# Kernel optimization log

Measured on AMD Instinct MI355X. Metric: run time of the kernel, lower is better.

The kernel has to match this reference:

```python
import jax, jax.numpy as jnp
import numpy as np

N, E, D_IN, HID, H = 50000, 800000, 128, 64, 2
C = HID  # per-head dim (out_channels)


def _lin_params(key, fan_in, fan_out):
    kw, kb = jax.random.split(key)
    s = 1.0 / np.sqrt(fan_in)
    W = jax.random.uniform(kw, (fan_in, fan_out), jnp.float32, -s, s)
    b = jax.random.uniform(kb, (fan_out,), jnp.float32, -s, s)
    return W, b


def setup_inputs() -> dict:
    key = jax.random.key(0)
    ks = jax.random.split(key, 14)
    x = jax.random.normal(ks[0], (N, D_IN), jnp.float32)
    edge_index = jax.random.randint(ks[1], (2, E), 0, N, jnp.int32)
    inp = {"x": x, "edge_index": edge_index}
    dims = [D_IN, HID, HID]
    i = 2
    for L, d_in in enumerate(dims, start=1):
        for nm, fo in (("q", H * C), ("k", H * C), ("v", H * C), ("s", HID)):
            W, b = _lin_params(ks[i], d_in, fo)
            inp[f"W{L}{nm}"] = W
            inp[f"b{L}{nm}"] = b
            i += 1
            if i >= 14:
                ks = jax.random.split(ks[-1], 14)
                i = 0
    return inp


def _transformer_conv(x, src, dst, Wq, bq, Wk, bk, Wv, bv, Ws, bs):
    # x: [N, d_in] -> out: [N, HID]
    q = (x @ Wq + bq).reshape(N, H, C)
    k = (x @ Wk + bk).reshape(N, H, C)
    v = (x @ Wv + bv).reshape(N, H, C)
    qi = q[dst]                      # [E, H, C] gather at destination (query)
    kj = k[src]                      # [E, H, C] gather at source (key)
    alpha = jnp.sum(qi * kj, axis=-1) / jnp.sqrt(jnp.float32(C))  # [E, H]
    amax = jax.ops.segment_max(alpha, dst, num_segments=N)        # [N, H]
    ex = jnp.exp(alpha - amax[dst])                               # [E, H]
    denom = jax.ops.segment_sum(ex, dst, num_segments=N)          # [N, H]
    attn = ex / (denom[dst] + 1e-16)                              # [E, H]
    msg = v[src] * attn[:, :, None]                               # [E, H, C]
    out = jax.ops.segment_sum(msg, dst, num_segments=N)           # [N, H, C]
    out = out.mean(axis=1)                                        # concat=False: head mean
    return out + x @ Ws + bs                                      # root skip


def reference(x, edge_index,
              W1q, b1q, W1k, b1k, W1v, b1v, W1s, b1s,
              W2q, b2q, W2k, b2k, W2v, b2v, W2s, b2s,
              W3q, b3q, W3k, b3k, W3v, b3v, W3s, b3s):
    src, dst = edge_index[0], edge_index[1]
    h = jax.nn.relu(_transformer_conv(x, src, dst, W1q, b1q, W1k, b1k, W1v, b1v, W1s, b1s))
    h = jax.nn.relu(_transformer_conv(h, src, dst, W2q, b2q, W2k, b2k, W2v, b2v, W2s, b2s))
    h = jax.nn.relu(_transformer_conv(h, src, dst, W3q, b3q, W3k, b3k, W3v, b3v, W3s, b3s))
    return h
```

## Files before the change

### kernel.cpp

```cpp
#include <hip/hip_runtime.h>
#include <cstdint>

typedef _Float16 f16;
typedef __attribute__((ext_vector_type(2))) _Float16 f16x2;
typedef __attribute__((ext_vector_type(4))) _Float16 f16x4;
typedef __attribute__((ext_vector_type(8))) _Float16 f16x8;
typedef __attribute__((ext_vector_type(4))) float f32x4;

#if defined(__has_builtin)
# if __has_builtin(__builtin_amdgcn_fdot2)
#  define HAVE_FDOT2 1
# endif
#endif


__global__ void hist_kernel(const int* __restrict__ dst, int* __restrict__ cnt, int E) {
    int e = blockIdx.x * blockDim.x + threadIdx.x;
    if (e < E) atomicAdd(&cnt[dst[e]], 1);
}

__global__ __launch_bounds__(256) void block_scan_kernel(
    const int* __restrict__ cnt, int* __restrict__ rowptr,
    int* __restrict__ partials, int n) {
    __shared__ int lds[256];
    int tid = threadIdx.x;
    int i = blockIdx.x * 256 + tid;
    int v = (i < n) ? cnt[i] : 0;
    lds[tid] = v;
    __syncthreads();
    for (int off = 1; off < 256; off <<= 1) {
        int t = (tid >= off) ? lds[tid - off] : 0;
        __syncthreads();
        lds[tid] += t;
        __syncthreads();
    }
    if (i < n) rowptr[i + 1] = lds[tid];
    if (tid == 255) partials[blockIdx.x] = lds[255];
}

__global__ __launch_bounds__(256) void partial_scan_kernel(int* __restrict__ partials, int nb) {
    __shared__ int lds[256];
    int tid = threadIdx.x;
    int v = (tid < nb) ? partials[tid] : 0;
    lds[tid] = v;
    __syncthreads();
    for (int off = 1; off < 256; off <<= 1) {
        int t = (tid >= off) ? lds[tid - off] : 0;
        __syncthreads();
        lds[tid] += t;
        __syncthreads();
    }
    if (tid < nb) partials[tid] = lds[tid] - v;
}

__global__ __launch_bounds__(256) void add_offsets_kernel(
    int* __restrict__ rowptr, const int* __restrict__ partials, int n) {
    int i = blockIdx.x * 256 + threadIdx.x;
    if (i < n) rowptr[i + 1] += partials[blockIdx.x];
    if (i == 0) rowptr[0] = 0;
}

__global__ void scatter_kernel(const int* __restrict__ src, const int* __restrict__ dst,
                               const int* __restrict__ rowptr, int* __restrict__ cnt,
                               int* __restrict__ src_sorted, int E) {
    int e = blockIdx.x * blockDim.x + threadIdx.x;
    if (e < E) {
        int d = dst[e];
        int p = rowptr[d] + atomicAdd(&cnt[d], 1);
        src_sorted[p] = src[e];
    }
}


__global__ __launch_bounds__(256) void prep_w_kernel(
    const float* __restrict__ Wq, const float* __restrict__ Wk,
    const float* __restrict__ Wv, const float* __restrict__ Ws,
    const float* __restrict__ bq, const float* __restrict__ bk,
    const float* __restrict__ bv, const float* __restrict__ bs,
    f16* __restrict__ Wt, float* __restrict__ bias, int K) {
    int idx = blockIdx.x * 256 + threadIdx.x;
    if (idx < 448) {
        bias[idx] = (idx < 128) ? bq[idx]
                  : (idx < 256) ? bk[idx - 128]
                  : (idx < 384) ? bv[idx - 256]
                  : bs[idx - 384];
    }
    if (idx >= 448 * K) return;
    int c = idx / K, k = idx - c * K;
    float v;
    if (c < 128)      v = Wq[k * 128 + c];
    else if (c < 256) v = Wk[k * 128 + (c - 128)];
    else if (c < 384) v = Wv[k * 128 + (c - 256)];
    else              v = Ws[k * 64 + (c - 384)];
    Wt[(size_t)c * K + k] = (f16)v;
}


template <int K, bool F32IN>
__global__ __launch_bounds__(256) void gemm_qkvs_kernel(
    const void* __restrict__ Xv, const f16* __restrict__ Wt,
    const float* __restrict__ bias, f16* __restrict__ out, int M) {
    __shared__ f16 xa[64 * K];
    __shared__ f16 wb[2][64 * K];
    int row0 = blockIdx.x * 64;
    int tid = threadIdx.x;
    constexpr int CPRW = K / 8;

    if (F32IN) {
        const float* X = (const float*)Xv;
        constexpr int CPR = K / 4;
        for (int c = tid; c < 64 * CPR; c += 256) {
            int r = c / CPR, kc = c % CPR;
            int gr = row0 + r;
            float4 v = {0.f, 0.f, 0.f, 0.f};
            if (gr < M) v = *(const float4*)(X + (size_t)gr * K + kc * 4);
            f16x4 hv = {(f16)v.x, (f16)v.y, (f16)v.z, (f16)v.w};
            int off = (r * K + kc * 4) * 2;
            off ^= (r & 7) << 4;
            *(f16x4*)((char*)xa + off) = hv;
        }
    } else {
        const f16* X = (const f16*)Xv;
        for (int c = tid; c < 64 * CPRW; c += 256) {
            int r = c / CPRW, kc = c % CPRW;
            int gr = row0 + r;
            uint4 v = {0, 0, 0, 0};
            if (gr < M) v = *(const uint4*)(X + (size_t)gr * K + kc * 8);
            int off = (r * K + kc * 8) * 2;
            off ^= (r & 7) << 4;
            *(uint4*)((char*)xa + off) = v;
        }
    }
    for (int c = tid; c < 64 * CPRW; c += 256) {
        int r = c / CPRW, kc = c % CPRW;
        uint4 v = *(const uint4*)(Wt + (size_t)r * K + kc * 8);
        int off = (r * K + kc * 8) * 2;
        off ^= (r & 7) << 4;
        *(uint4*)((char*)wb[0] + off) = v;
    }
    __syncthreads();

    int lane = tid & 63, wid = tid >> 6;
    int fr = lane & 15, fk = lane >> 4;
    int arow = wid * 16 + fr;
    constexpr int NK = K / 32;
    f16x8 af[NK];
    #pragma unroll
    for (int ks = 0; ks < NK; ++ks) {
        int aoff = (arow * K + ks * 32 + fk * 8) * 2;
        aoff ^= (arow & 7) << 4;
        af[ks] = *(f16x8*)((char*)xa + aoff);
    }

    int orow = row0 + wid * 16 + fk * 4;
    for (int ct = 0; ct < 7; ++ct) {
        if (ct < 6) {
            int col0 = (ct + 1) * 64;
            f16* dstb = wb[(ct + 1) & 1];
            for (int c = tid; c < 64 * CPRW; c += 256) {
                int r = c / CPRW, kc = c % CPRW;
                uint4 v = *(const uint4*)(Wt + (size_t)(col0 + r) * K + kc * 8);
                int off = (r * K + kc * 8) * 2;
                off ^= (r & 7) << 4;
                *(uint4*)((char*)dstb + off) = v;
            }
        }

        const f16* curb = wb[ct & 1];
        f32x4 acc[4] = {};
        #pragma unroll
        for (int ks = 0; ks < NK; ++ks) {
            #pragma unroll
            for (int cf = 0; cf < 4; ++cf) {
                int brow = cf * 16 + fr;
                int boff = (brow * K + ks * 32 + fk * 8) * 2;
                boff ^= (brow & 7) << 4;
                f16x8 bf = *(f16x8*)((char*)curb + boff);
                acc[cf] = __builtin_amdgcn_mfma_f32_16x16x32_f16(af[ks], bf, acc[cf], 0, 0, 0);
            }
        }

        int ocol = ct * 64 + fr;
        #pragma unroll
        for (int cf = 0; cf < 4; ++cf) {
            float b = bias[ocol + cf * 16];
            #pragma unroll
            for (int r = 0; r < 4; ++r) {
                int gr = orow + r;
                if (gr < M) out[(size_t)gr * 448 + ocol + cf * 16] = (f16)(acc[cf][r] + b);
            }
        }
        __syncthreads();
    }
}


__global__ __launch_bounds__(256) void attn_kernel(
    const f16* __restrict__ T,
    const int* __restrict__ rowptr, const int* __restrict__ srcs,
    f16* __restrict__ hout, float* __restrict__ fout, int n, int final_layer) {
    int node = blockIdx.x * 4 + (threadIdx.x >> 6);
    if (node >= n) return;
    int lane = threadIdx.x & 63;
    int c8 = lane & 7, eg = lane >> 3;
    const size_t base = (size_t)node * 448;
    const int co = c8 * 8;

    f16x8 q0 = *(const f16x8*)(T + base + co);
    f16x8 q1 = *(const f16x8*)(T + base + 64 + co);
    float m0 = -__builtin_inff(), m1 = -__builtin_inff();
    float s0 = 0.f, s1 = 0.f;
    float av0[8] = {}, av1[8] = {};

    int beg = rowptr[node], end = rowptr[node + 1];
    if (beg < end) {
        int nsrc = srcs[min(beg + eg, end - 1)];
        for (int i0 = beg; i0 < end; i0 += 8) {
            int i = i0 + eg;
            bool valid = (i < end);
            int sidx = nsrc;
            if (i0 + 8 < end) nsrc = srcs[min(i + 8, end - 1)];

            const f16* p = T + (size_t)sidx * 448 + co;
            f16x8 k0 = *(const f16x8*)(p + 128);
            f16x8 k1 = *(const f16x8*)(p + 192);
            f16x8 v0 = *(const f16x8*)(p + 256);
            f16x8 v1 = *(const f16x8*)(p + 320);

            float d0 = 0.f, d1 = 0.f;
#ifdef HAVE_FDOT2
            #pragma unroll
            for (int j = 0; j < 4; ++j) {
                f16x2 a0 = {q0[2 * j], q0[2 * j + 1]};
                f16x2 b0 = {k0[2 * j], k0[2 * j + 1]};
                d0 = __builtin_amdgcn_fdot2(a0, b0, d0, false);
                f16x2 a1 = {q1[2 * j], q1[2 * j + 1]};
                f16x2 b1 = {k1[2 * j], k1[2 * j + 1]};
                d1 = __builtin_amdgcn_fdot2(a1, b1, d1, false);
            }
#else
            #pragma unroll
            for (int j = 0; j < 8; ++j) {
                d0 += (float)q0[j] * (float)k0[j];
                d1 += (float)q1[j] * (float)k1[j];
            }
#endif
            d0 += __shfl_xor(d0, 1); d1 += __shfl_xor(d1, 1);
            d0 += __shfl_xor(d0, 2); d1 += __shfl_xor(d1, 2);
            d0 += __shfl_xor(d0, 4); d1 += __shfl_xor(d1, 4);
            d0 *= 0.125f; d1 *= 0.125f;
            if (!valid) { d0 = -__builtin_inff(); d1 = -__builtin_inff(); }

            if (__any(d0 > m0 + 6.f || d1 > m1 + 6.f)) {
                float t0 = d0, t1 = d1;
                t0 = fmaxf(t0, __shfl_xor(t0, 8));  t1 = fmaxf(t1, __shfl_xor(t1, 8));
                t0 = fmaxf(t0, __shfl_xor(t0, 16)); t1 = fmaxf(t1, __shfl_xor(t1, 16));
                t0 = fmaxf(t0, __shfl_xor(t0, 32)); t1 = fmaxf(t1, __shfl_xor(t1, 32));
                float nm0 = fmaxf(m0, t0), nm1 = fmaxf(m1, t1);
                float f0 = __expf(m0 - nm0), f1 = __expf(m1 - nm1);
                s0 *= f0; s1 *= f1;
                #pragma unroll
                for (int j = 0; j < 8; ++j) { av0[j] *= f0; av1[j] *= f1; }
                m0 = nm0; m1 = nm1;
            }
            float p0 = __expf(d0 - m0);
            float p1 = __expf(d1 - m1);
            s0 += p0; s1 += p1;
            #pragma unroll
            for (int j = 0; j < 8; ++j) {
                av0[j] += p0 * (float)v0[j];
                av1[j] += p1 * (float)v1[j];
            }
        }
    }

    s0 += __shfl_xor(s0, 8);  s1 += __shfl_xor(s1, 8);
    s0 += __shfl_xor(s0, 16); s1 += __shfl_xor(s1, 16);
    s0 += __shfl_xor(s0, 32); s1 += __shfl_xor(s1, 32);
    float inv0 = 1.0f / (s0 + 1e-16f), inv1 = 1.0f / (s1 + 1e-16f);
    float r[8];
    #pragma unroll
    for (int j = 0; j < 8; ++j) {
        float a0 = av0[j], a1 = av1[j];
        a0 += __shfl_xor(a0, 8);  a1 += __shfl_xor(a1, 8);
        a0 += __shfl_xor(a0, 16); a1 += __shfl_xor(a1, 16);
        a0 += __shfl_xor(a0, 32); a1 += __shfl_xor(a1, 32);
        r[j] = 0.5f * (a0 * inv0 + a1 * inv1);
    }

    if (lane < 8) {
        f16x8 sk = *(const f16x8*)(T + base + 384 + co);
        #pragma unroll
        for (int j = 0; j < 8; ++j) r[j] = fmaxf(r[j] + (float)sk[j], 0.f);
        if (final_layer) {
            float4* dst4 = (float4*)(fout + (size_t)node * 64 + co);
            dst4[0] = make_float4(r[0], r[1], r[2], r[3]);
            dst4[1] = make_float4(r[4], r[5], r[6], r[7]);
        } else {
            f16x8 o = {(f16)r[0], (f16)r[1], (f16)r[2], (f16)r[3],
                       (f16)r[4], (f16)r[5], (f16)r[6], (f16)r[7]};
            *(f16x8*)(hout + (size_t)node * 64 + co) = o;
        }
    }
}


extern "C" void kernel_launch(void* const* d_in, const int* in_sizes, int n_in,
                              void* d_out, int out_size, void* d_ws, size_t ws_size,
                              hipStream_t stream) {
    const float* x = (const float*)d_in[0];
    const int* ei  = (const int*)d_in[1];
    const int N = in_sizes[0] / 128;
    const int E = in_sizes[1] / 2;
    const int* src = ei;
    const int* dst = ei + E;

    const float* Wq[3] = {(const float*)d_in[2],  (const float*)d_in[10], (const float*)d_in[18]};
    const float* bq[3] = {(const float*)d_in[3],  (const float*)d_in[11], (const float*)d_in[19]};
    const float* Wk[3] = {(const float*)d_in[4],  (const float*)d_in[12], (const float*)d_in[20]};
    const float* bk[3] = {(const float*)d_in[5],  (const float*)d_in[13], (const float*)d_in[21]};
    const float* Wv[3] = {(const float*)d_in[6],  (const float*)d_in[14], (const float*)d_in[22]};
    const float* bv[3] = {(const float*)d_in[7],  (const float*)d_in[15], (const float*)d_in[23]};
    const float* Wsk[3]= {(const float*)d_in[8],  (const float*)d_in[16], (const float*)d_in[24]};
    const float* bsk[3]= {(const float*)d_in[9],  (const float*)d_in[17], (const float*)d_in[25]};

    char* p = (char*)d_ws;
    int* rowptr   = (int*)p; p += (size_t)(N + 1) * 4;
    int* cnt      = (int*)p; p += (size_t)N * 4;
    int* srcs     = (int*)p; p += (size_t)E * 4;
    int* partials = (int*)p; p += 256 * 4;
    p = (char*)(((uintptr_t)p + 255) & ~(uintptr_t)255);
    f16* Xh   = (f16*)p; p += (size_t)N * 64 * 2;
    f16* QKVS = (f16*)p; p += (size_t)N * 448 * 2;
    f16* Wt0  = (f16*)p; p += (size_t)448 * 128 * 2;
    f16* Wt1  = (f16*)p; p += (size_t)448 * 64 * 2;
    f16* Wt2  = (f16*)p; p += (size_t)448 * 64 * 2;
    float* bias0 = (float*)p; p += 448 * 4;
    float* bias1 = (float*)p; p += 448 * 4;
    float* bias2 = (float*)p; p += 448 * 4;
    if ((size_t)(p - (char*)d_ws) > ws_size) return;

    f16* Wt[3] = {Wt0, Wt1, Wt2};
    float* bias[3] = {bias0, bias1, bias2};

    for (int l = 0; l < 3; ++l) {
        int K = (l == 0) ? 128 : 64;
        prep_w_kernel<<<(448 * K + 255) / 256, 256, 0, stream>>>(
            Wq[l], Wk[l], Wv[l], Wsk[l], bq[l], bk[l], bv[l], bsk[l], Wt[l], bias[l], K);
    }

    int nb = (N + 255) / 256;
    hipMemsetAsync(cnt, 0, (size_t)N * 4, stream);
    hist_kernel<<<(E + 255) / 256, 256, 0, stream>>>(dst, cnt, E);
    block_scan_kernel<<<nb, 256, 0, stream>>>(cnt, rowptr, partials, N);
    partial_scan_kernel<<<1, 256, 0, stream>>>(partials, nb);
    add_offsets_kernel<<<nb, 256, 0, stream>>>(rowptr, partials, N);
    hipMemsetAsync(cnt, 0, (size_t)N * 4, stream);
    scatter_kernel<<<(E + 255) / 256, 256, 0, stream>>>(src, dst, rowptr, cnt, srcs, E);

    int gx = (N + 63) / 64;
    for (int l = 0; l < 3; ++l) {
        if (l == 0)
            gemm_qkvs_kernel<128, true><<<gx, 256, 0, stream>>>(x, Wt[l], bias[l], QKVS, N);
        else
            gemm_qkvs_kernel<64, false><<<gx, 256, 0, stream>>>(Xh, Wt[l], bias[l], QKVS, N);
        attn_kernel<<<(N + 3) / 4, 256, 0, stream>>>(
            QKVS, rowptr, srcs, Xh, (float*)d_out, N, (l == 2) ? 1 : 0);
    }
}
```

Baseline: 380.3 us.

## Prepack weights in MFMA fragment order and load GEMM operands directly from global

The weight prep kernel now writes W in the exact per-lane MFMA fragment order, so each wave can fetch its B fragments with one contiguous 16-byte load per lane straight from global/L2. The GEMM also loads A fragments straight from global, with the fp32-to-fp16 conversion done in registers. Together these remove all LDS staging, the swizzles and the block barriers. The weights (448×K fp16) are small and shared by every block, so they should stay in cache. The risk is that each wave now re-reads all weights through L1/L2 instead of sharing one LDS copy, and A loads become row-strided rather than coalesced.

```diff
diff --git a/kernel.cpp b/kernel.cpp
--- a/kernel.cpp
+++ b/kernel.cpp
@@ -3,7 +3,6 @@
 
 typedef _Float16 f16;
 typedef __attribute__((ext_vector_type(2))) _Float16 f16x2;
-typedef __attribute__((ext_vector_type(4))) _Float16 f16x4;
 typedef __attribute__((ext_vector_type(8))) _Float16 f16x8;
 typedef __attribute__((ext_vector_type(4))) float f32x4;
 
@@ -77,7 +76,7 @@
     const float* __restrict__ Wv, const float* __restrict__ Ws,
     const float* __restrict__ bq, const float* __restrict__ bk,
     const float* __restrict__ bv, const float* __restrict__ bs,
-    f16* __restrict__ Wt, float* __restrict__ bias, int K) {
+    f16* __restrict__ Wf, float* __restrict__ bias, int K) {
     int idx = blockIdx.x * 256 + threadIdx.x;
     if (idx < 448) {
         bias[idx] = (idx < 128) ? bq[idx]
@@ -92,105 +91,64 @@
     else if (c < 256) v = Wk[k * 128 + (c - 128)];
     else if (c < 384) v = Wv[k * 128 + (c - 256)];
     else              v = Ws[k * 64 + (c - 384)];
-    Wt[(size_t)c * K + k] = (f16)v;
+    int NK = K >> 5;
+    int ct = c >> 6, cf = (c >> 4) & 3, fr = c & 15;
+    int ks = k >> 5, fk = (k >> 3) & 3, j = k & 7;
+    size_t off = ((size_t)(((ct * 4 + cf) * NK + ks) * 4 + fk) * 16 + fr) * 8 + j;
+    Wf[off] = (f16)v;
 }
 
 
 template <int K, bool F32IN>
 __global__ __launch_bounds__(256) void gemm_qkvs_kernel(
-    const void* __restrict__ Xv, const f16* __restrict__ Wt,
+    const void* __restrict__ Xv, const f16* __restrict__ Wf,
     const float* __restrict__ bias, f16* __restrict__ out, int M) {
-    __shared__ f16 xa[64 * K];
-    __shared__ f16 wb[2][64 * K];
-    int row0 = blockIdx.x * 64;
+    constexpr int NK = K / 32;
     int tid = threadIdx.x;
-    constexpr int CPRW = K / 8;
-
-    if (F32IN) {
-        const float* X = (const float*)Xv;
-        constexpr int CPR = K / 4;
-        for (int c = tid; c < 64 * CPR; c += 256) {
-            int r = c / CPR, kc = c % CPR;
-            int gr = row0 + r;
-            float4 v = {0.f, 0.f, 0.f, 0.f};
-            if (gr < M) v = *(const float4*)(X + (size_t)gr * K + kc * 4);
-            f16x4 hv = {(f16)v.x, (f16)v.y, (f16)v.z, (f16)v.w};
-            int off = (r * K + kc * 4) * 2;
-            off ^= (r & 7) << 4;
-            *(f16x4*)((char*)xa + off) = hv;
-        }
-    } else {
-        const f16* X = (const f16*)Xv;
-        for (int c = tid; c < 64 * CPRW; c += 256) {
-            int r = c / CPRW, kc = c % CPRW;
-            int gr = row0 + r;
-            uint4 v = {0, 0, 0, 0};
-            if (gr < M) v = *(const uint4*)(X + (size_t)gr * K + kc * 8);
-            int off = (r * K + kc * 8) * 2;
-            off ^= (r & 7) << 4;
-            *(uint4*)((char*)xa + off) = v;
-        }
-    }
-    for (int c = tid; c < 64 * CPRW; c += 256) {
-        int r = c / CPRW, kc = c % CPRW;
-        uint4 v = *(const uint4*)(Wt + (size_t)r * K + kc * 8);
-        int off = (r * K + kc * 8) * 2;
-        off ^= (r & 7) << 4;
-        *(uint4*)((char*)wb[0] + off) = v;
-    }
-    __syncthreads();
-
     int lane = tid & 63, wid = tid >> 6;
     int fr = lane & 15, fk = lane >> 4;
-    int arow = wid * 16 + fr;
-    constexpr int NK = K / 32;
+    int arow = blockIdx.x * 64 + wid * 16 + fr;
+    int crow = (arow < M) ? arow : (M - 1);
+
     f16x8 af[NK];
-    #pragma unroll
-    for (int ks = 0; ks < NK; ++ks) {
-        int aoff = (arow * K + ks * 32 + fk * 8) * 2;
-        aoff ^= (arow & 7) << 4;
-        af[ks] = *(f16x8*)((char*)xa + aoff);
-    }
-
-    int orow = row0 + wid * 16 + fk * 4;
+    if (F32IN) {
+        const float* X = (const float*)Xv + (size_t)crow * K;
+        #pragma unroll
+        for (int ks = 0; ks < NK; ++ks) {
+            float4 lo = *(const float4*)(X + ks * 32 + fk * 8);
+            float4 hi = *(const float4*)(X + ks * 32 + fk * 8 + 4);
+            af[ks] = {(f16)lo.x, (f16)lo.y, (f16)lo.z, (f16)lo.w,
+                      (f16)hi.x, (f16)hi.y, (f16)hi.z, (f16)hi.w};
+        }
+    } else {
+        const f16* X = (const f16*)Xv + (size_t)crow * K;
+        #pragma unroll
+        for (int ks = 0; ks < NK; ++ks)
+            af[ks] = *(const f16x8*)(X + ks * 32 + fk * 8);
+    }
+
+    int orow0 = blockIdx.x * 64 + wid * 16 + fk * 4;
     for (int ct = 0; ct < 7; ++ct) {
-        if (ct < 6) {
-            int col0 = (ct + 1) * 64;
-            f16* dstb = wb[(ct + 1) & 1];
-            for (int c = tid; c < 64 * CPRW; c += 256) {
-                int r = c / CPRW, kc = c % CPRW;
-                uint4 v = *(const uint4*)(Wt + (size_t)(col0 + r) * K + kc * 8);
-                int off = (r * K + kc * 8) * 2;
-                off ^= (r & 7) << 4;
-                *(uint4*)((char*)dstb + off) = v;
-            }
-        }
-
-        const f16* curb = wb[ct & 1];
         f32x4 acc[4] = {};
         #pragma unroll
-        for (int ks = 0; ks < NK; ++ks) {
-            #pragma unroll
-            for (int cf = 0; cf < 4; ++cf) {
-                int brow = cf * 16 + fr;
-                int boff = (brow * K + ks * 32 + fk * 8) * 2;
-                boff ^= (brow & 7) << 4;
-                f16x8 bf = *(f16x8*)((char*)curb + boff);
+        for (int cf = 0; cf < 4; ++cf) {
+            const f16* Wp = Wf + (size_t)(ct * 4 + cf) * NK * 512 + (size_t)lane * 8;
+            #pragma unroll
+            for (int ks = 0; ks < NK; ++ks) {
+                f16x8 bf = *(const f16x8*)(Wp + (size_t)ks * 512);
                 acc[cf] = __builtin_amdgcn_mfma_f32_16x16x32_f16(af[ks], bf, acc[cf], 0, 0, 0);
             }
         }
-
         int ocol = ct * 64 + fr;
         #pragma unroll
         for (int cf = 0; cf < 4; ++cf) {
             float b = bias[ocol + cf * 16];
             #pragma unroll
             for (int r = 0; r < 4; ++r) {
-                int gr = orow + r;
+                int gr = orow0 + r;
                 if (gr < M) out[(size_t)gr * 448 + ocol + cf * 16] = (f16)(acc[cf][r] + b);
             }
         }
-        __syncthreads();
     }
 }
 
```

Result: faster. 358.6 us (-5.7%).
